# Kernel tuning notes

Measured on AMD Instinct MI355X. Metric: run time of the kernel, lower is better.

## Reference

```python
import jax, jax.numpy as jnp
import numpy as np

N = 50000
E = 800000
D = 64  # in = hidden = out channels


def _graph_conv(x, src, dst, ew, W_rel, b_rel, W_root, b_root, num_nodes):
    # PyG GraphConv: out = lin_rel(scatter_add(x[src] * w -> dst)) + lin_root(x)
    msg = x[src] * ew[:, None]                      # [E, d_in] edge-wise gather
    agg = jax.ops.segment_sum(msg, dst, num_segments=num_nodes)  # scatter-add
    return agg @ W_rel.T + b_rel + x @ W_root.T + b_root


def setup_inputs() -> dict:
    key = jax.random.key(0)
    ks = jax.random.split(key, 16)
    s = 0.05
    inp = {
        "X": jax.random.normal(ks[0], (N, D), dtype=jnp.float32),
        "edge_index": jax.random.randint(ks[1], (2, E), 0, N, dtype=jnp.int64),
        "edge_weight": jax.random.uniform(ks[2], (E,), dtype=jnp.float32),
        # conv_whx_x: in -> hidden
        "Wrel1": jax.random.normal(ks[3], (D, D), dtype=jnp.float32) * s,
        "brel1": jax.random.normal(ks[4], (D,), dtype=jnp.float32) * s,
        "Wroot1": jax.random.normal(ks[5], (D, D), dtype=jnp.float32) * s,
        "broot1": jax.random.normal(ks[6], (D,), dtype=jnp.float32) * s,
        # conv_whh_hs1: hidden -> hidden
        "Wrel2": jax.random.normal(ks[7], (D, D), dtype=jnp.float32) * s,
        "brel2": jax.random.normal(ks[8], (D,), dtype=jnp.float32) * s,
        "Wroot2": jax.random.normal(ks[9], (D, D), dtype=jnp.float32) * s,
        "broot2": jax.random.normal(ks[10], (D,), dtype=jnp.float32) * s,
        # conv_wy_y: hidden -> out
        "Wrel3": jax.random.normal(ks[11], (D, D), dtype=jnp.float32) * s,
        "brel3": jax.random.normal(ks[12], (D,), dtype=jnp.float32) * s,
        "Wroot3": jax.random.normal(ks[13], (D, D), dtype=jnp.float32) * s,
        "broot3": jax.random.normal(ks[14], (D,), dtype=jnp.float32) * s,
    }
    return inp


def reference(X, edge_index, edge_weight,
              Wrel1, brel1, Wroot1, broot1,
              Wrel2, brel2, Wroot2, broot2,
              Wrel3, brel3, Wroot3, broot3):
    num_nodes = X.shape[0]
    src, dst = edge_index[0], edge_index[1]
    # first call: hidden state H_{t-1} = zeros(N, out_channels)
    H_prev = jnp.zeros((num_nodes, D), dtype=X.dtype)
    Whx_x = _graph_conv(X, src, dst, edge_weight, Wrel1, brel1, Wroot1, broot1, num_nodes)
    Whh_h = _graph_conv(H_prev, src, dst, edge_weight, Wrel2, brel2, Wroot2, broot2, num_nodes)
    H = jax.nn.sigmoid(Whx_x + Whh_h)
    Wy_h = _graph_conv(H, src, dst, edge_weight, Wrel3, brel3, Wroot3, broot3, num_nodes)
    return jax.nn.sigmoid(Wy_h)
```

## Files before the change

### kernel.cpp

```cpp
#include <hip/hip_runtime.h>

#define D 64
#define CAP 64

typedef unsigned short u16;
typedef unsigned int u32;
typedef short bf16x8 __attribute__((ext_vector_type(8)));
typedef float f32x4 __attribute__((ext_vector_type(4)));

__device__ __forceinline__ u16 f2bf(float f) {
    u32 u = __float_as_uint(f);
    return (u16)((u + 0x7FFFu + ((u >> 16) & 1u)) >> 16);
}

__global__ void k_prep(const float* __restrict__ X, u16* __restrict__ Xbf,
                       int* __restrict__ cnt, int n4, int N,
                       const float* __restrict__ Wrel1, const float* __restrict__ Wroot1,
                       const float* __restrict__ Wrel3, const float* __restrict__ Wroot3,
                       const float* __restrict__ brel1, const float* __restrict__ broot1,
                       const float* __restrict__ brel2, const float* __restrict__ broot2,
                       const float* __restrict__ brel3, const float* __restrict__ broot3,
                       u16* __restrict__ Wpk, float* __restrict__ Bpk) {
    int i = blockIdx.x * blockDim.x + threadIdx.x;
    if (i < N) cnt[i] = 0;

    if (i < 2048) {
        int f    = i >> 6;
        int lane = i & 63;
        int stage = f >> 4, rest = f & 15;
        int mat = rest >> 3, t = (rest >> 1) & 3, kk = rest & 1;
        int ml = lane & 15, ql = lane >> 4;
        const float* W = stage ? (mat ? Wroot3 : Wrel3) : (mat ? Wroot1 : Wrel1);
        const float* src = W + (t * 16 + ml) * D + kk * 32 + ql * 8;
        union { u16 h[8]; uint4 v; } o;
#pragma unroll
        for (int e = 0; e < 8; ++e) o.h[e] = f2bf(src[e]);
        *reinterpret_cast<uint4*>(Wpk + (size_t)(f * 64 + lane) * 8) = o.v;
    }
    if (i < 128) {
        int stage = i >> 6, c = i & 63;
        Bpk[i] = stage ? (brel3[c] + broot3[c])
                       : (brel1[c] + broot1[c] + brel2[c] + broot2[c]);
    }

    if (i >= n4) return;
    float4 v = reinterpret_cast<const float4*>(X)[i];
    ushort4 o;
    o.x = f2bf(v.x); o.y = f2bf(v.y); o.z = f2bf(v.z); o.w = f2bf(v.w);
    reinterpret_cast<ushort4*>(Xbf)[i] = o;
}

__global__ void k_fill(const int* __restrict__ ei, const float* __restrict__ ew,
                       int* __restrict__ cnt, u32* __restrict__ pairs,
                       int E, int step) {
    const int g  = blockIdx.x & 7;
    const int b  = blockIdx.x >> 3;
    const int lo = g * step;
    const int hi = lo + step;
    const int nthr = (gridDim.x >> 3) * blockDim.x;
    const int t  = b * blockDim.x + threadIdx.x;
    const int nchunk = E >> 2;

    for (int c = t; c < nchunk; c += nthr) {
        int e = c * 4;
        int4 d4 = *reinterpret_cast<const int4*>(ei + E + e);
#define DO_EDGE(dd, kk)                                                          \
        if ((dd) >= lo && (dd) < hi) {                                           \
            int p = atomicAdd(cnt + (dd), 1);                                    \
            if (p < CAP)                                                         \
                pairs[(dd) * CAP + p] =                                          \
                    (((u32)f2bf(ew[e + kk])) << 16) | (u32)ei[e + kk];           \
        }
        DO_EDGE(d4.x, 0)
        DO_EDGE(d4.y, 1)
        DO_EDGE(d4.z, 2)
        DO_EDGE(d4.w, 3)
#undef DO_EDGE
    }
    if (g == 0 && t == 0) {
        for (int e = nchunk * 4; e < E; ++e) {
            int d = ei[E + e];
            int p = atomicAdd(cnt + d, 1);
            if (p < CAP) pairs[d * CAP + p] = (((u32)f2bf(ew[e])) << 16) | (u32)ei[e];
        }
    }
}

template <int STAGE>
__global__ __launch_bounds__(256, 3) void k_stage(
        const u16* __restrict__ Gbf,
        const u16* __restrict__ Wpk,
        const float* __restrict__ Bpk,
        const int* __restrict__ cnt, const u32* __restrict__ pairs,
        float* __restrict__ outF, u16* __restrict__ outBf, int N) {
    __shared__ __align__(16) u16 smem[4 * 8 * 72];
    const int lane = threadIdx.x & 63;
    const int wid  = threadIdx.x >> 6;
    const int ml   = lane & 15;
    const int ql   = lane >> 4;
    const int hq   = lane & 15;
    const int n0   = blockIdx.x * 32 + wid * 8;
    u16* sw = smem + wid * 8 * 72;

    if (n0 >= N) return;

    int cidx = n0 + (lane & 7); if (cidx >= N) cidx = N - 1;
    const int cnt8 = cnt[cidx];

    int deg[8], degmax = 0;
#pragma unroll
    for (int i = 0; i < 8; ++i) {
        int d = (n0 + i < N) ? __builtin_amdgcn_readlane(cnt8, i) : 0;
        if (d > CAP) d = CAP;
        deg[i] = d;
        degmax = degmax > d ? degmax : d;
    }

    u32 pp[8];
#pragma unroll
    for (int i = 0; i < 8; ++i) {
        int r = n0 + i; if (r >= N) r = N - 1;
        pp[i] = (lane < deg[i]) ? pairs[(size_t)r * CAP + lane] : 0u;
    }

    const bool qb0 = (ql & 1) != 0;
    const bool qb1 = (ql & 2) != 0;
    const int  hq8 = hq * 8;
    const char* gbase = (const char*)Gbf;

    f32x4 acc[2];
#pragma unroll
    for (int p = 0; p < 2; ++p) acc[p] = (f32x4){0.f, 0.f, 0.f, 0.f};

    uint2 vA[4][2], vB[4][2], vC[4][2];
    u32   wA[4][2], wB[4][2], wC[4][2];
#define ISSUE(vbuf, wbuf, jj)                                                   \
    _Pragma("unroll") for (int s = 0; s < 4; ++s)                               \
    _Pragma("unroll") for (int p = 0; p < 2; ++p) {                             \
        u32 r0 = (u32)__builtin_amdgcn_readlane((int)pp[4 * p + 0], (jj) + s);  \
        u32 r1 = (u32)__builtin_amdgcn_readlane((int)pp[4 * p + 1], (jj) + s);  \
        u32 r2 = (u32)__builtin_amdgcn_readlane((int)pp[4 * p + 2], (jj) + s);  \
        u32 r3 = (u32)__builtin_amdgcn_readlane((int)pp[4 * p + 3], (jj) + s);  \
        u32 c01 = qb0 ? r1 : r0;                                                \
        u32 c23 = qb0 ? r3 : r2;                                                \
        u32 sel = qb1 ? c23 : c01;                                              \
        wbuf[s][p] = sel;                                                       \
        vbuf[s][p] = *(const uint2*)(gbase + ((size_t)(sel & 0xFFFFu) << 7) + hq8); \
    }
#define CONSUME(vbuf, wbuf)                                                     \
    _Pragma("unroll") for (int s = 0; s < 4; ++s)                               \
    _Pragma("unroll") for (int p = 0; p < 2; ++p) {                             \
        float w  = __uint_as_float(wbuf[s][p] & 0xFFFF0000u);                   \
        uint2 d  = vbuf[s][p];                                                  \
        acc[p][0] = fmaf(w, __uint_as_float(d.x << 16),         acc[p][0]);     \
        acc[p][1] = fmaf(w, __uint_as_float(d.x & 0xFFFF0000u), acc[p][1]);     \
        acc[p][2] = fmaf(w, __uint_as_float(d.y << 16),         acc[p][2]);     \
        acc[p][3] = fmaf(w, __uint_as_float(d.y & 0xFFFF0000u), acc[p][3]);     \
    }

    if (degmax > 0) {
        int j = 0;
        ISSUE(vA, wA, 0)
        if (4 < degmax) ISSUE(vB, wB, 4)
        for (;;) {
            if (j + 8 < degmax) ISSUE(vC, wC, j + 8)
            CONSUME(vA, wA)
            j += 4;
            if (j >= degmax) break;
            if (j + 8 < degmax) ISSUE(vA, wA, j + 8)
            CONSUME(vB, wB)
            j += 4;
            if (j >= degmax) break;
            if (j + 8 < degmax) ISSUE(vB, wB, j + 8)
            CONSUME(vC, wC)
            j += 4;
            if (j >= degmax) break;
        }
    }
#undef ISSUE
#undef CONSUME

#pragma unroll
    for (int p = 0; p < 2; ++p) {
        uint2 packed;
        packed.x = ((u32)f2bf(acc[p][1]) << 16) | (u32)f2bf(acc[p][0]);
        packed.y = ((u32)f2bf(acc[p][3]) << 16) | (u32)f2bf(acc[p][2]);
        int row = 4 * p + ql;
        *reinterpret_cast<uint2*>(sw + row * 72 + hq * 4) = packed;
    }

    bf16x8 brel[4][2], broot[4][2];
#pragma unroll
    for (int t = 0; t < 4; ++t)
#pragma unroll
        for (int kk = 0; kk < 2; ++kk) {
            brel[t][kk]  = *reinterpret_cast<const bf16x8*>(Wpk + (size_t)(((0 * 4 + t) * 2 + kk) * 64 + lane) * 8);
            broot[t][kk] = *reinterpret_cast<const bf16x8*>(Wpk + (size_t)(((1 * 4 + t) * 2 + kk) * 64 + lane) * 8);
        }

    const int am = ml & 7;
    bf16x8 a_agg[2], a_x[2];
#pragma unroll
    for (int kk = 0; kk < 2; ++kk)
        a_agg[kk] = *reinterpret_cast<bf16x8*>(sw + am * 72 + kk * 32 + ql * 8);
    {
        int r = n0 + am; if (r >= N) r = N - 1;
#pragma unroll
        for (int kk = 0; kk < 2; ++kk)
            a_x[kk] = *reinterpret_cast<const bf16x8*>(Gbf + (size_t)r * D + kk * 32 + ql * 8);
    }

#pragma unroll
    for (int t = 0; t < 4; ++t) {
        int c = t * 16 + ml;
        float bias = Bpk[c];

        f32x4 accv = {0.f, 0.f, 0.f, 0.f};
        accv = __builtin_amdgcn_mfma_f32_16x16x32_bf16(a_agg[0], brel[t][0],  accv, 0, 0, 0);
        accv = __builtin_amdgcn_mfma_f32_16x16x32_bf16(a_agg[1], brel[t][1],  accv, 0, 0, 0);
        accv = __builtin_amdgcn_mfma_f32_16x16x32_bf16(a_x[0],   broot[t][0], accv, 0, 0, 0);
        accv = __builtin_amdgcn_mfma_f32_16x16x32_bf16(a_x[1],   broot[t][1], accv, 0, 0, 0);
        if (ql < 2) {
#pragma unroll
            for (int r = 0; r < 4; ++r) {
                int row = n0 + ql * 4 + r;
                if (row < N) {
                    float z = accv[r] + bias;
                    float h = 1.f / (1.f + __expf(-z));
                    int off = row * D + c;
                    if (STAGE == 1) outBf[off] = f2bf(h);
                    else            outF[off]  = h;
                }
            }
        }
    }
}

extern "C" void kernel_launch(void* const* d_in, const int* in_sizes, int n_in,
                              void* d_out, int out_size, void* d_ws, size_t ws_size,
                              hipStream_t stream) {
    const float* X      = (const float*)d_in[0];
    const int*   ei     = (const int*)  d_in[1];
    const float* ew     = (const float*)d_in[2];
    const float* Wrel1  = (const float*)d_in[3];
    const float* brel1  = (const float*)d_in[4];
    const float* Wroot1 = (const float*)d_in[5];
    const float* broot1 = (const float*)d_in[6];
    const float* brel2  = (const float*)d_in[8];
    const float* broot2 = (const float*)d_in[10];
    const float* Wrel3  = (const float*)d_in[11];
    const float* brel3  = (const float*)d_in[12];
    const float* Wroot3 = (const float*)d_in[13];
    const float* broot3 = (const float*)d_in[14];

    const int N = in_sizes[0] / D;
    const int E = in_sizes[1] / 2;

    char* ws = (char*)d_ws;
    int* cnt = (int*)ws;
    size_t off = (((size_t)N * 4) + 255) & ~(size_t)255;
    u32* pairs = (u32*)(ws + off);        off += (size_t)N * CAP * 4;
    u16* Xbf   = (u16*)(ws + off);        off += (size_t)N * D * 2;
    u16* Hbf   = (u16*)(ws + off);        off += (size_t)N * D * 2;
    u16* Wpk   = (u16*)(ws + off);        off += (size_t)32 * 64 * 8 * 2;
    float* Bpk = (float*)(ws + off);

    {
        int n4 = N * D / 4;
        int T  = n4 > N ? n4 : N;
        k_prep<<<(T + 255) / 256, 256, 0, stream>>>(
            X, Xbf, cnt, n4, N, Wrel1, Wroot1, Wrel3, Wroot3,
            brel1, broot1, brel2, broot2, brel3, broot3, Wpk, Bpk);
    }
    {
        int step = (N + 7) / 8;
        k_fill<<<1600, 256, 0, stream>>>(ei, ew, cnt, pairs, E, step);
    }

    const int NB = (N + 31) / 32;
    k_stage<1><<<NB, 256, 0, stream>>>(Xbf, Wpk, Bpk,
                                       cnt, pairs, nullptr, Hbf, N);
    k_stage<2><<<NB, 256, 0, stream>>>(Hbf, Wpk + 16 * 64 * 8, Bpk + 64,
                                       cnt, pairs, (float*)d_out, nullptr, N);
}
```

Before: 200.0 us.

## Stage edge records in LDS and gather 16-byte bf16 rows per lane

The gather loop now writes each node's packed (weight, src) edge records into shared memory and reads four at a time with 128-bit LDS loads. This replaces the per-edge readlane/select chains. Each lane now owns one node and one 8-channel slice and fetches 16 bytes per neighbour row instead of 8. Each lane accumulates 8 channels across 4 edges per stage. This lowers the scalar readlane overhead and doubles the width of each memory request. The cost is extra LDS traffic, more vector registers for the buffers, and possibly lower occupancy.

```diff
diff --git a/kernel.cpp b/kernel.cpp
--- a/kernel.cpp
+++ b/kernel.cpp
@@ -94,13 +94,16 @@
         const int* __restrict__ cnt, const u32* __restrict__ pairs,
         float* __restrict__ outF, u16* __restrict__ outBf, int N) {
     __shared__ __align__(16) u16 smem[4 * 8 * 72];
+    __shared__ __align__(16) u32 recs[4 * 8 * 68];
     const int lane = threadIdx.x & 63;
     const int wid  = threadIdx.x >> 6;
     const int ml   = lane & 15;
     const int ql   = lane >> 4;
-    const int hq   = lane & 15;
+    const int o    = lane >> 3;
+    const int c    = lane & 7;
     const int n0   = blockIdx.x * 32 + wid * 8;
     u16* sw = smem + wid * 8 * 72;
+    u32* rw = recs + wid * 8 * 68;
 
     if (n0 >= N) return;
 
@@ -116,77 +119,76 @@
         degmax = degmax > d ? degmax : d;
     }
 
-    u32 pp[8];
 #pragma unroll
     for (int i = 0; i < 8; ++i) {
         int r = n0 + i; if (r >= N) r = N - 1;
-        pp[i] = (lane < deg[i]) ? pairs[(size_t)r * CAP + lane] : 0u;
-    }
-
-    const bool qb0 = (ql & 1) != 0;
-    const bool qb1 = (ql & 2) != 0;
-    const int  hq8 = hq * 8;
+        u32 pv = (lane < deg[i]) ? pairs[(size_t)r * CAP + lane] : 0u;
+        rw[i * 68 + lane] = pv;
+    }
+
+    const u32* prow  = rw + o * 68;
     const char* gbase = (const char*)Gbf;
-
-    f32x4 acc[2];
-#pragma unroll
-    for (int p = 0; p < 2; ++p) acc[p] = (f32x4){0.f, 0.f, 0.f, 0.f};
-
-    uint2 vA[4][2], vB[4][2], vC[4][2];
-    u32   wA[4][2], wB[4][2], wC[4][2];
-#define ISSUE(vbuf, wbuf, jj)                                                   \
-    _Pragma("unroll") for (int s = 0; s < 4; ++s)                               \
-    _Pragma("unroll") for (int p = 0; p < 2; ++p) {                             \
-        u32 r0 = (u32)__builtin_amdgcn_readlane((int)pp[4 * p + 0], (jj) + s);  \
-        u32 r1 = (u32)__builtin_amdgcn_readlane((int)pp[4 * p + 1], (jj) + s);  \
-        u32 r2 = (u32)__builtin_amdgcn_readlane((int)pp[4 * p + 2], (jj) + s);  \
-        u32 r3 = (u32)__builtin_amdgcn_readlane((int)pp[4 * p + 3], (jj) + s);  \
-        u32 c01 = qb0 ? r1 : r0;                                                \
-        u32 c23 = qb0 ? r3 : r2;                                                \
-        u32 sel = qb1 ? c23 : c01;                                              \
-        wbuf[s][p] = sel;                                                       \
-        vbuf[s][p] = *(const uint2*)(gbase + ((size_t)(sel & 0xFFFFu) << 7) + hq8); \
-    }
-#define CONSUME(vbuf, wbuf)                                                     \
-    _Pragma("unroll") for (int s = 0; s < 4; ++s)                               \
-    _Pragma("unroll") for (int p = 0; p < 2; ++p) {                             \
-        float w  = __uint_as_float(wbuf[s][p] & 0xFFFF0000u);                   \
-        uint2 d  = vbuf[s][p];                                                  \
-        acc[p][0] = fmaf(w, __uint_as_float(d.x << 16),         acc[p][0]);     \
-        acc[p][1] = fmaf(w, __uint_as_float(d.x & 0xFFFF0000u), acc[p][1]);     \
-        acc[p][2] = fmaf(w, __uint_as_float(d.y << 16),         acc[p][2]);     \
-        acc[p][3] = fmaf(w, __uint_as_float(d.y & 0xFFFF0000u), acc[p][3]);     \
+    const int  c16   = c * 16;
+
+    float acc[8];
+#pragma unroll
+    for (int k = 0; k < 8; ++k) acc[k] = 0.f;
+
+    uint4 rA, rB, rC;
+    uint4 vA[4], vB[4], vC[4];
+#define RECQ(rg, jj)  rg = *reinterpret_cast<const uint4*>(prow + (jj));
+#define ISSUEV(vg, rg)                                                          \
+    _Pragma("unroll") for (int s = 0; s < 4; ++s) {                             \
+        u32 rec = (s == 0) ? (rg).x : (s == 1) ? (rg).y : (s == 2) ? (rg).z : (rg).w; \
+        vg[s] = *reinterpret_cast<const uint4*>(                                \
+            gbase + ((size_t)(rec & 0xFFFFu) << 7) + c16);                      \
+    }
+#define CONSUME(vg, rg)                                                         \
+    _Pragma("unroll") for (int s = 0; s < 4; ++s) {                             \
+        u32 rec = (s == 0) ? (rg).x : (s == 1) ? (rg).y : (s == 2) ? (rg).z : (rg).w; \
+        float w  = __uint_as_float(rec & 0xFFFF0000u);                          \
+        uint4 d  = vg[s];                                                       \
+        acc[0] = fmaf(w, __uint_as_float(d.x << 16),         acc[0]);           \
+        acc[1] = fmaf(w, __uint_as_float(d.x & 0xFFFF0000u), acc[1]);           \
+        acc[2] = fmaf(w, __uint_as_float(d.y << 16),         acc[2]);           \
+        acc[3] = fmaf(w, __uint_as_float(d.y & 0xFFFF0000u), acc[3]);           \
+        acc[4] = fmaf(w, __uint_as_float(d.z << 16),         acc[4]);           \
+        acc[5] = fmaf(w, __uint_as_float(d.z & 0xFFFF0000u), acc[5]);           \
+        acc[6] = fmaf(w, __uint_as_float(d.w << 16),         acc[6]);           \
+        acc[7] = fmaf(w, __uint_as_float(d.w & 0xFFFF0000u), acc[7]);           \
     }
 
     if (degmax > 0) {
+        RECQ(rA, 0)
+        ISSUEV(vA, rA)
+        if (4 < degmax) { RECQ(rB, 4) ISSUEV(vB, rB) }
         int j = 0;
-        ISSUE(vA, wA, 0)
-        if (4 < degmax) ISSUE(vB, wB, 4)
         for (;;) {
-            if (j + 8 < degmax) ISSUE(vC, wC, j + 8)
-            CONSUME(vA, wA)
+            if (j + 8 < degmax) { RECQ(rC, j + 8) ISSUEV(vC, rC) }
+            CONSUME(vA, rA)
             j += 4;
             if (j >= degmax) break;
-            if (j + 8 < degmax) ISSUE(vA, wA, j + 8)
-            CONSUME(vB, wB)
+            if (j + 8 < degmax) { RECQ(rA, j + 8) ISSUEV(vA, rA) }
+            CONSUME(vB, rB)
             j += 4;
             if (j >= degmax) break;
-            if (j + 8 < degmax) ISSUE(vB, wB, j + 8)
-            CONSUME(vC, wC)
+            if (j + 8 < degmax) { RECQ(rB, j + 8) ISSUEV(vB, rB) }
+            CONSUME(vC, rC)
             j += 4;
             if (j >= degmax) break;
         }
     }
-#undef ISSUE
+#undef RECQ
+#undef ISSUEV
 #undef CONSUME
 
-#pragma unroll
-    for (int p = 0; p < 2; ++p) {
-        uint2 packed;
-        packed.x = ((u32)f2bf(acc[p][1]) << 16) | (u32)f2bf(acc[p][0]);
-        packed.y = ((u32)f2bf(acc[p][3]) << 16) | (u32)f2bf(acc[p][2]);
-        int row = 4 * p + ql;
-        *reinterpret_cast<uint2*>(sw + row * 72 + hq * 4) = packed;
+    {
+        uint4 packed;
+        packed.x = ((u32)f2bf(acc[1]) << 16) | (u32)f2bf(acc[0]);
+        packed.y = ((u32)f2bf(acc[3]) << 16) | (u32)f2bf(acc[2]);
+        packed.z = ((u32)f2bf(acc[5]) << 16) | (u32)f2bf(acc[4]);
+        packed.w = ((u32)f2bf(acc[7]) << 16) | (u32)f2bf(acc[6]);
+        *reinterpret_cast<uint4*>(sw + o * 72 + c * 8) = packed;
     }
 
     bf16x8 brel[4][2], broot[4][2];
@@ -212,8 +214,8 @@
 
 #pragma unroll
     for (int t = 0; t < 4; ++t) {
-        int c = t * 16 + ml;
-        float bias = Bpk[c];
+        int ch = t * 16 + ml;
+        float bias = Bpk[ch];
 
         f32x4 accv = {0.f, 0.f, 0.f, 0.f};
         accv = __builtin_amdgcn_mfma_f32_16x16x32_bf16(a_agg[0], brel[t][0],  accv, 0, 0, 0);
@@ -227,7 +229,7 @@
                 if (row < N) {
                     float z = accv[r] + bias;
                     float h = 1.f / (1.f + __expf(-z));
-                    int off = row * D + c;
+                    int off = row * D + ch;
                     if (STAGE == 1) outBf[off] = f2bf(h);
                     else            outF[off]  = h;
                 }
```

Result: faster. 188.7 us (-5.7%).
